# Kernel optimization log

Hardware: AMD Instinct MI355X
Metric: run time of the kernel (lower is better)

Reference implementation:

```python
import jax, jax.numpy as jnp
import numpy as np
from jax import lax

BS = 256

def layer_norm(x, w, b, eps=1e-5):
    mu = jnp.mean(x, axis=-1, keepdims=True)
    var = jnp.mean((x - mu) ** 2, axis=-1, keepdims=True)
    return (x - mu) / jnp.sqrt(var + eps) * w + b

def conv2d(x, w, b):
    y = lax.conv_general_dilated(x, w, (1, 1), 'VALID', dimension_numbers=('NCHW', 'OIHW', 'NCHW'))
    return y + b[None, :, None, None]

def max_pool2(x):
    return lax.reduce_window(x, -jnp.inf, lax.max, (1, 1, 2, 2), (1, 1, 2, 2), 'VALID')

def mha(x, wqkv, bqkv, wo, bo, nheads):
    # x: (L, B, E); torch nn.MultiheadAttention in eval mode (dropout off)
    L, B, E = x.shape
    hd = E // nheads
    qkv = jnp.einsum('lbd,ed->lbe', x, wqkv) + bqkv
    q, k, v = jnp.split(qkv, 3, axis=-1)
    q = q.reshape(L, B, nheads, hd) * (hd ** -0.5)
    k = k.reshape(L, B, nheads, hd)
    v = v.reshape(L, B, nheads, hd)
    att = jax.nn.softmax(jnp.einsum('qbhd,kbhd->bhqk', q, k), axis=-1)
    o = jnp.einsum('bhqk,kbhd->qbhd', att, v).reshape(L, B, E)
    return jnp.einsum('lbe,oe->lbo', o, wo) + bo

def grouped_mha(u, wqkv, bqkv, wo, bo, nheads):
    # u: (G, L, B, E) -- the 16 distinct small MHA blocks batched into one grouped attention
    G, L, B, E = u.shape
    hd = E // nheads
    qkv = jnp.einsum('glbd,ged->glbe', u, wqkv) + bqkv[:, None, None, :]
    q, k, v = jnp.split(qkv, 3, axis=-1)
    q = q.reshape(G, L, B, nheads, hd) * (hd ** -0.5)
    k = k.reshape(G, L, B, nheads, hd)
    v = v.reshape(G, L, B, nheads, hd)
    att = jax.nn.softmax(jnp.einsum('gqbhd,gkbhd->gbhqk', q, k), axis=-1)
    o = jnp.einsum('gbhqk,gkbhd->gqbhd', att, v).reshape(G, L, B, E)
    return jnp.einsum('glbe,goe->glbo', o, wo) + bo[:, None, None, :]

def setup_inputs() -> dict:
    key = jax.random.key(0)
    ks = iter(jax.random.split(key, 40))
    n = lambda shape, s=0.02: jax.random.normal(next(ks), shape, dtype=jnp.float32) * s
    inp = {
        't': jax.random.uniform(next(ks), (BS, 128, 128), dtype=jnp.float32) * 255.0,
        'conv1_w': n((32, 1, 3, 3), 0.1), 'conv1_b': n((32,)),
        'conv2_w': n((32, 32, 3, 3), 0.05), 'conv2_b': n((32,)),
        'expand_w': n((64, 36), 0.05), 'expand_b': n((64,)),
        'mha_wqkv': n((16, 192, 64)), 'mha_bqkv': n((16, 192)),
        'mha_wo': n((16, 64, 64)), 'mha_bo': n((16, 64)),
        'ln1_w': jnp.ones((64,), jnp.float32), 'ln1_b': jnp.zeros((64,), jnp.float32),
        'enc_wqkv': n((3 * 2048, 2048)), 'enc_bqkv': n((3 * 2048,)),
        'enc_wo': n((2048, 2048)), 'enc_bo': n((2048,)),
        'enc_ln1_w': jnp.ones((2048,), jnp.float32), 'enc_ln1_b': jnp.zeros((2048,), jnp.float32),
        'enc_w1': n((2048, 2048)), 'enc_b1': n((2048,)),
        'enc_w2': n((2048, 2048)), 'enc_b2': n((2048,)),
        'enc_ln2_w': jnp.ones((2048,), jnp.float32), 'enc_ln2_b': jnp.zeros((2048,), jnp.float32),
        'f1_w': n((512, 16 * 2048), 0.01), 'f1_b': n((512,)),
        'f2_w': n((128, 512)), 'f2_b': n((128,)),
        'f3_w': n((25, 128)), 'f3_b': n((25,)),
    }
    return inp

def reference(t, conv1_w, conv1_b, conv2_w, conv2_b, expand_w, expand_b,
              mha_wqkv, mha_bqkv, mha_wo, mha_bo, ln1_w, ln1_b,
              enc_wqkv, enc_bqkv, enc_wo, enc_bo, enc_ln1_w, enc_ln1_b,
              enc_w1, enc_b1, enc_w2, enc_b2, enc_ln2_w, enc_ln2_b,
              f1_w, f1_b, f2_w, f2_b, f3_w, f3_b):
    bs = t.shape[0]
    t = t / 255.0
    # 4x4 grid of 32x32 tiles -> (bs*16, 1, 32, 32); replaces the double python loop
    x = t.reshape(bs, 4, 32, 4, 32).transpose(0, 1, 3, 2, 4).reshape(bs * 16, 1, 32, 32)
    u = max_pool2(conv2d(x, conv1_w, conv1_b))   # (bs*16, 32, 15, 15)
    u = max_pool2(conv2d(u, conv2_w, conv2_b))   # (bs*16, 32, 6, 6)
    u = u.reshape(bs * 16, 32, 36)
    u = jax.nn.relu(u @ expand_w.T + expand_b)
    u = u.reshape(16, 32, bs, 64)                 # raw reshape, exactly as in source
    att = grouped_mha(u, mha_wqkv, mha_bqkv, mha_wo, mha_bo, 4)
    u = layer_norm(u + att, ln1_w, ln1_b)         # dropout is identity in eval
    x = u.reshape(16, bs, 2048)
    # TransformerEncoderLayer d_model=2048, nhead=16, post-norm, ReLU FFN (eval)
    a = mha(x, enc_wqkv, enc_bqkv, enc_wo, enc_bo, 16)
    x = layer_norm(x + a, enc_ln1_w, enc_ln1_b)
    ff = jax.nn.relu(x @ enc_w1.T + enc_b1) @ enc_w2.T + enc_b2
    x = layer_norm(x + ff, enc_ln2_w, enc_ln2_b)
    u = x.reshape(bs, 16 * 2048)                  # raw reshape, exactly as in source
    u = jax.nn.relu(u @ f1_w.T + f1_b)
    u = jax.nn.relu(u @ f2_w.T + f2_b)
    return u @ f3_w.T + f3_b
```

## Files before the change

### kernel.cpp

```cpp
#include <hip/hip_runtime.h>


#define EPS 1e-5f

typedef __attribute__((ext_vector_type(8))) short s16x8;
typedef __attribute__((ext_vector_type(4))) float f32x4;

__device__ inline float bf2f(ushort u) {
    union { unsigned u; float f; } x; x.u = ((unsigned)u) << 16; return x.f;
}
__device__ inline ushort f2bf(float f) {
    union { float f; unsigned u; } x; x.f = f;
    unsigned r = x.u + 0x7FFFu + ((x.u >> 16) & 1u);
    return (ushort)(r >> 16);
}
__device__ inline void gload_lds16(const void* g, void* l) {
    __builtin_amdgcn_global_load_lds(
        (const __attribute__((address_space(1))) unsigned int*)g,
        (__attribute__((address_space(3))) unsigned int*)l, 16, 0, 0);
}

__global__ __launch_bounds__(256) void conv1_pool(
    const float* __restrict__ t, const float* __restrict__ w,
    const float* __restrict__ bias, ushort* __restrict__ out)
{
    __shared__ float tile[32][33];
    __shared__ float ws9[288];
    __shared__ float bs[32];
    int n = blockIdx.x, tid = threadIdx.x;
    int b = n >> 4, tt = n & 15, ty = tt >> 2, tx = tt & 3;
    const float* tb = t + (long)b * 16384 + ty * 32 * 128 + tx * 32;
    for (int i = tid; i < 1024; i += 256) {
        int r = i >> 5, cc = i & 31;
        tile[r][cc] = tb[r * 128 + cc] * (1.0f / 255.0f);
    }
    for (int i = tid; i < 288; i += 256) ws9[i] = w[i];
    if (tid < 32) bs[tid] = bias[tid];
    __syncthreads();
    for (int o = tid; o < 7200; o += 256) {
        int c = o / 225, p = o - c * 225;
        int py = p / 15, px = p - py * 15;
        float in[4][4];
        #pragma unroll
        for (int iy = 0; iy < 4; ++iy) {
            #pragma unroll
            for (int ix = 0; ix < 4; ++ix) in[iy][ix] = tile[py * 2 + iy][px * 2 + ix];
        }
        float b0 = bs[c];
        float a00 = b0, a01 = b0, a10 = b0, a11 = b0;
        const float* wc = &ws9[c * 9];
        #pragma unroll
        for (int ky = 0; ky < 3; ++ky) {
            #pragma unroll
            for (int kx = 0; kx < 3; ++kx) {
                float wv = wc[ky * 3 + kx];
                a00 += in[ky][kx] * wv;     a01 += in[ky][kx + 1] * wv;
                a10 += in[ky + 1][kx] * wv; a11 += in[ky + 1][kx + 1] * wv;
            }
        }
        out[(long)n * 7200 + o] = f2bf(fmaxf(fmaxf(a00, a01), fmaxf(a10, a11)));
    }
}

__global__ __launch_bounds__(256) void convw_prep(
    const float* __restrict__ w, ushort* __restrict__ wk)
{
    int i = blockIdx.x * 256 + threadIdx.x;
    if (i >= 9216) return;
    int kz = i >> 10, rem = i & 1023;
    int oc = rem >> 5, ci = rem & 31;
    wk[i] = f2bf(w[oc * 288 + ci * 9 + kz]);
}

__global__ __launch_bounds__(256) void conv2_mfma(
    const ushort* __restrict__ u1, const ushort* __restrict__ wk,
    const float* __restrict__ bias, float* __restrict__ u2)
{
    __shared__ __align__(16) ushort tiles[2][7680];
    __shared__ float hp[2][2376];
    int tid = threadIdx.x;
    int wave = tid >> 6, lane = tid & 63;
    int n0 = blockIdx.x * 2;

    for (int u = tid; u < 1800; u += 256) {
        int img = u / 900, v = u - img * 900;
        int ks = v / 225, pos = v - ks * 225;
        int y = pos / 15, x = pos - y * 15;
        const ushort* src = u1 + (long)(n0 + img) * 7200 + (ks * 8) * 225 + pos;
        union { s16x8 v8; ushort us[8]; } pk;
        #pragma unroll
        for (int j = 0; j < 8; ++j) pk.us[j] = src[j * 225];
        int r = y * 16 + x;
        int chunk = ks ^ ((r >> 1) & 3);
        *(s16x8*)((char*)&tiles[img][0] + r * 64 + (chunk << 4)) = pk.v8;
    }
    __syncthreads();

    int img = wave >> 1, nf = wave & 1;
    int fr = lane & 15, ks4 = lane >> 4;
    int rb[9];
    #pragma unroll
    for (int m = 0; m < 9; ++m) {
        int pos = m * 16 + fr;
        int py = pos / 12, px = pos - py * 12;
        rb[m] = py * 16 + px;
    }
    f32x4 acc[9];
    #pragma unroll
    for (int m = 0; m < 9; ++m) acc[m] = (f32x4){0.f, 0.f, 0.f, 0.f};
    const char* tbase = (const char*)&tiles[img][0];
    #pragma unroll
    for (int kz = 0; kz < 9; ++kz) {
        int ky = kz / 3, kx = kz - ky * 3;
        s16x8 bf = *(const s16x8*)(wk + kz * 1024 + (nf * 16 + fr) * 32 + ks4 * 8);
        #pragma unroll
        for (int m = 0; m < 9; ++m) {
            int r = rb[m] + ky * 16 + kx;
            s16x8 af = *(const s16x8*)(tbase + r * 64 + ((ks4 ^ ((r >> 1) & 3)) << 4));
            acc[m] = __builtin_amdgcn_mfma_f32_16x16x32_bf16(af, bf, acc[m], 0, 0, 0);
        }
    }

    int oc = nf * 16 + fr;
    int cr4 = ks4 * 4;
    #pragma unroll
    for (int m = 0; m < 9; ++m) {
        float v01 = fmaxf(acc[m][0], acc[m][1]);
        float v23 = fmaxf(acc[m][2], acc[m][3]);
        int p0 = m * 16 + cr4;
        int py = p0 / 12, px0 = p0 - py * 12;
        int rowb = py * 6 + (px0 >> 1);
        hp[img][rowb * 33 + oc] = v01;
        hp[img][(rowb + 1) * 33 + oc] = v23;
    }
    __syncthreads();

    for (int u = tid; u < 2304; u += 256) {
        int im = u / 1152, v = u - im * 1152;
        int o = v / 36, opos = v - o * 36;
        int i = opos / 6, jj = opos - i * 6;
        float a = hp[im][((2 * i) * 6 + jj) * 33 + o];
        float b = hp[im][((2 * i + 1) * 6 + jj) * 33 + o];
        u2[(long)(n0 + im) * 1152 + o * 36 + opos] = fmaxf(a, b) + bias[o];
    }
}

__global__ __launch_bounds__(256) void expand_k(
    const float* __restrict__ u2, const float* __restrict__ w,
    const float* __restrict__ bias, float* __restrict__ out)
{
    __shared__ float ws[2304];
    __shared__ float xs[2304];
    __shared__ float bs[64];
    int tid = threadIdx.x;
    long r0 = (long)blockIdx.x * 64;
    const float* src = u2 + r0 * 36;
    for (int i = tid; i < 2304; i += 256) { ws[i] = w[i]; xs[i] = src[i]; }
    if (tid < 64) bs[tid] = bias[tid];
    __syncthreads();
    int row = tid >> 2, qq = tid & 3;
    float x[36];
    #pragma unroll
    for (int k4 = 0; k4 < 36; k4 += 4) *(float4*)&x[k4] = *(const float4*)&xs[row * 36 + k4];
    float res[16];
    #pragma unroll
    for (int eo = 0; eo < 16; ++eo) {
        int e = qq * 16 + eo;
        const float* wr = &ws[e * 36];
        float acc = bs[e];
        #pragma unroll
        for (int k4 = 0; k4 < 36; k4 += 4) {
            float4 wv = *(const float4*)&wr[k4];
            acc += x[k4] * wv.x + x[k4 + 1] * wv.y + x[k4 + 2] * wv.z + x[k4 + 3] * wv.w;
        }
        res[eo] = fmaxf(acc, 0.0f);
    }
    float* orow = out + (r0 + row) * 64 + qq * 16;
    #pragma unroll
    for (int v4 = 0; v4 < 4; ++v4) *(float4*)(orow + v4 * 4) = *(float4*)&res[v4 * 4];
}

template <int BM, int BN, int BK, int TM, int TN, int ACT, int SPLITK>
__global__ __launch_bounds__(256) void gemm_tn(
    const float* __restrict__ A, const float* __restrict__ B,
    const float* __restrict__ bias, float* __restrict__ C,
    int M, int N, int K, int lda, int ldb, int ldc,
    long sA, long sB, long sBias, long sC)
{
    constexpr int NTX = BN / TN;
    constexpr int KG = BK / 4;
    __shared__ float As[BK][BM + 4];
    __shared__ float Bs[BK][BN + 4];
    int tid = threadIdx.x;
    int tx = tid % NTX, ty = tid / NTX;
    int n0 = blockIdx.x * BN, m0 = blockIdx.y * BM;
    int bz = blockIdx.z;
    int batch = bz / SPLITK, kz = bz - batch * SPLITK;
    int Kc = K / SPLITK;
    int k0 = kz * Kc, k1 = k0 + Kc;
    A += (long)batch * sA; B += (long)batch * sB; C += (long)batch * sC;
    const float* bp = bias ? bias + (long)batch * sBias : nullptr;
    float acc[TM][TN] = {};
    for (int kt = k0; kt < k1; kt += BK) {
        constexpr int A4 = BM * BK / 4;
        #pragma unroll
        for (int e0 = 0; e0 < A4; e0 += 256) {
            int e = e0 + tid;
            int rr = e / KG, kg = (e - rr * KG) * 4;
            int gm = m0 + rr;
            float4 v = make_float4(0.f, 0.f, 0.f, 0.f);
            if (gm < M) v = *(const float4*)(A + (long)gm * lda + kt + kg);
            As[kg + 0][rr] = v.x; As[kg + 1][rr] = v.y; As[kg + 2][rr] = v.z; As[kg + 3][rr] = v.w;
        }
        constexpr int B4 = BN * BK / 4;
        #pragma unroll
        for (int e0 = 0; e0 < B4; e0 += 256) {
            int e = e0 + tid;
            int rr = e / KG, kg = (e - rr * KG) * 4;
            int gn = n0 + rr;
            float4 v = make_float4(0.f, 0.f, 0.f, 0.f);
            if (gn < N) v = *(const float4*)(B + (long)gn * ldb + kt + kg);
            Bs[kg + 0][rr] = v.x; Bs[kg + 1][rr] = v.y; Bs[kg + 2][rr] = v.z; Bs[kg + 3][rr] = v.w;
        }
        __syncthreads();
        #pragma unroll
        for (int k = 0; k < BK; ++k) {
            float a[TM], b[TN];
            #pragma unroll
            for (int i = 0; i < TM; i += 4) *(float4*)&a[i] = *(const float4*)&As[k][ty * TM + i];
            #pragma unroll
            for (int j = 0; j < TN; j += 4) *(float4*)&b[j] = *(const float4*)&Bs[k][tx * TN + j];
            #pragma unroll
            for (int i = 0; i < TM; ++i) {
                #pragma unroll
                for (int j = 0; j < TN; ++j) acc[i][j] += a[i] * b[j];
            }
        }
        __syncthreads();
    }
    #pragma unroll
    for (int i = 0; i < TM; ++i) {
        int gm = m0 + ty * TM + i;
        if (gm < M) {
            #pragma unroll
            for (int j = 0; j < TN; ++j) {
                int gn = n0 + tx * TN + j;
                if (gn < N) {
                    float v = acc[i][j];
                    if (SPLITK > 1) {
                        atomicAdd(&C[(long)gm * ldc + gn], v);
                    } else {
                        if (bp) v += bp[gn];
                        if (ACT == 1) v = fmaxf(v, 0.0f);
                        C[(long)gm * ldc + gn] = v;
                    }
                }
            }
        }
    }
}

template <int ACT, int OUT_MODE, int SPLITK = 1>
__global__ __launch_bounds__(256) void gemm_bf16(
    const ushort* __restrict__ A, const ushort* __restrict__ B,
    const float* __restrict__ bias, float* __restrict__ Cf,
    ushort* __restrict__ Cb, int M, int N, int K)
{
    __shared__ __align__(16) ushort As[8192];
    __shared__ __align__(16) ushort Bs[8192];
    int tid = threadIdx.x;
    int wave = tid >> 6, lane = tid & 63;
    int m0 = blockIdx.y * 128, n0 = blockIdx.x * 128;
    const ushort* ga = A + (long)(m0 + wave * 32 + (lane >> 3)) * K + (lane & 7) * 8;
    const ushort* gb = B + (long)(n0 + wave * 32 + (lane >> 3)) * K + (lane & 7) * 8;
    ushort* la = &As[wave * 2048];
    ushort* lb = &Bs[wave * 2048];
    int wr = wave >> 1, wc = wave & 1;
    int fr = lane & 15, ks = (lane >> 4) * 8;
    f32x4 acc[4][4];
    #pragma unroll
    for (int i = 0; i < 4; ++i)
        #pragma unroll
        for (int j = 0; j < 4; ++j) acc[i][j] = (f32x4){0.f, 0.f, 0.f, 0.f};

    int k0 = 0, k1 = K;
    if (SPLITK > 1) { int Kc = K / SPLITK; k0 = blockIdx.z * Kc; k1 = k0 + Kc; }
    for (int kt = k0; kt < k1; kt += 64) {
        #pragma unroll
        for (int i = 0; i < 4; ++i) {
            gload_lds16(ga + kt + (long)i * 8 * K, la + i * 512);
            gload_lds16(gb + kt + (long)i * 8 * K, lb + i * 512);
        }
        __syncthreads();
        #pragma unroll
        for (int kk = 0; kk < 64; kk += 32) {
            s16x8 af[4], bfr[4];
            #pragma unroll
            for (int m = 0; m < 4; ++m)
                af[m] = *(const s16x8*)&As[(wr * 64 + m * 16 + fr) * 64 + kk + ks];
            #pragma unroll
            for (int n = 0; n < 4; ++n)
                bfr[n] = *(const s16x8*)&Bs[(wc * 64 + n * 16 + fr) * 64 + kk + ks];
            #pragma unroll
            for (int m = 0; m < 4; ++m)
                #pragma unroll
                for (int n = 0; n < 4; ++n)
                    acc[m][n] = __builtin_amdgcn_mfma_f32_16x16x32_bf16(
                        af[m], bfr[n], acc[m][n], 0, 0, 0);
        }
        __syncthreads();
    }
    int cr = (lane >> 4) * 4;
    #pragma unroll
    for (int n = 0; n < 4; ++n) {
        int col = n0 + wc * 64 + n * 16 + fr;
        float bv = (SPLITK == 1 && bias) ? bias[col] : 0.f;
        #pragma unroll
        for (int m = 0; m < 4; ++m) {
            #pragma unroll
            for (int j = 0; j < 4; ++j) {
                int row = m0 + wr * 64 + m * 16 + cr + j;
                float v = acc[m][n][j] + bv;
                if (SPLITK > 1) {
                    Cf[(long)blockIdx.z * M * N + (long)row * N + col] = v;
                } else {
                    if (ACT == 1) v = fmaxf(v, 0.f);
                    if (OUT_MODE != 2) Cf[(long)row * N + col] = v;
                    if (OUT_MODE != 0) Cb[(long)row * N + col] = f2bf(v);
                }
            }
        }
    }
}

__global__ __launch_bounds__(256) void f1_reduce(
    const float* __restrict__ part, const float* __restrict__ bias,
    float* __restrict__ out)
{
    int i = blockIdx.x * 256 + threadIdx.x;
    float s = 0.f;
    #pragma unroll 8
    for (int k = 0; k < 64; ++k) s += part[(long)k * 131072 + i];
    out[i] = fmaxf(s + bias[i & 511], 0.f);
}

__global__ __launch_bounds__(256) void f2b_kernel(
    const float* __restrict__ in, ushort* __restrict__ out, int n8)
{
    int i = blockIdx.x * 256 + threadIdx.x;
    if (i >= n8) return;
    long base = (long)i * 8;
    float4 v0 = *(const float4*)(in + base);
    float4 v1 = *(const float4*)(in + base + 4);
    ushort4 a, b;
    a.x = f2bf(v0.x); a.y = f2bf(v0.y); a.z = f2bf(v0.z); a.w = f2bf(v0.w);
    b.x = f2bf(v1.x); b.y = f2bf(v1.y); b.z = f2bf(v1.z); b.w = f2bf(v1.w);
    *(ushort4*)(out + base) = a;
    *(ushort4*)(out + base + 4) = b;
}

__global__ __launch_bounds__(256) void gatt_ln(
    const float* __restrict__ qkv, const float* __restrict__ u,
    const float* __restrict__ wo, const float* __restrict__ bo,
    const float* __restrict__ lnw, const float* __restrict__ lnb,
    ushort* __restrict__ out)
{
    __shared__ float sm[12928];
    float* qs  = sm;
    float* ks  = sm + 2112;
    float* vs  = sm + 4160;
    float* wos = sm + 6208;
    float* os  = sm + 10560;
    float* psT = sm;
    float* bos = sm + 12736;
    float* lws = sm + 12800;
    float* lbs = sm + 12864;
    int gb = blockIdx.x;
    int g = gb >> 8, b = gb & 255;
    int tid = threadIdx.x;

    const float* base = qkv + (long)g * 1572864 + b * 192;
    for (int e = tid; e < 1536; e += 256) {
        int s = e / 48, c4 = (e - s * 48) * 4;
        float4 v = *(const float4*)(base + (long)s * 49152 + c4);
        if (c4 < 64) {
            float* q = &qs[s * 66 + c4];
            q[0] = v.x * 0.25f; q[1] = v.y * 0.25f; q[2] = v.z * 0.25f; q[3] = v.w * 0.25f;
        } else if (c4 < 128) {
            *(float4*)&ks[s * 64 + (c4 - 64)] = v;
        } else {
            *(float4*)&vs[s * 64 + (c4 - 128)] = v;
        }
    }
    const float* wog = wo + g * 4096;
    for (int i = tid; i < 4096; i += 256) wos[(i >> 6) * 68 + (i & 63)] = wog[i];
    if (tid < 64) { bos[tid] = bo[g * 64 + tid]; lws[tid] = lnw[tid]; lbs[tid] = lnb[tid]; }
    __syncthreads();

    int hr = tid >> 1;
    int h = hr >> 5, qi = hr & 31, half = tid & 1;
    float qreg[16];
    #pragma unroll
    for (int d2 = 0; d2 < 16; d2 += 2)
        *(float2*)&qreg[d2] = *(const float2*)&qs[qi * 66 + h * 16 + d2];
    float sc[16];
    #pragma unroll
    for (int jj = 0; jj < 16; ++jj) {
        int j = half * 16 + jj;
        const float* kr = &ks[j * 64 + h * 16];
        float a = 0.f;
        #pragma unroll
        for (int d4 = 0; d4 < 16; d4 += 4) {
            float4 kv = *(const float4*)&kr[d4];
            a += qreg[d4] * kv.x + qreg[d4 + 1] * kv.y + qreg[d4 + 2] * kv.z + qreg[d4 + 3] * kv.w;
        }
        sc[jj] = a;
    }
    float mx = sc[0];
    #pragma unroll
    for (int jj = 1; jj < 16; ++jj) mx = fmaxf(mx, sc[jj]);
    mx = fmaxf(mx, __shfl_xor(mx, 1));
    float sum = 0.f;
    #pragma unroll
    for (int jj = 0; jj < 16; ++jj) { sc[jj] = __expf(sc[jj] - mx); sum += sc[jj]; }
    sum += __shfl_xor(sum, 1);
    float inv = 1.0f / sum;
    __syncthreads();
    #pragma unroll
    for (int jj = 0; jj < 16; ++jj)
        psT[(half * 16 + jj) * 128 + h * 32 + qi] = sc[jj] * inv;
    __syncthreads();

    int si = tid >> 3, e0 = (tid & 7) * 8;
    int hh = e0 >> 4;
    float oacc[8] = {};
    for (int j = 0; j < 32; ++j) {
        float pj = psT[j * 128 + hh * 32 + si];
        const float* vr = &vs[j * 64 + e0];
        float4 v0 = *(const float4*)&vr[0];
        float4 v1 = *(const float4*)&vr[4];
        oacc[0] += pj * v0.x; oacc[1] += pj * v0.y; oacc[2] += pj * v0.z; oacc[3] += pj * v0.w;
        oacc[4] += pj * v1.x; oacc[5] += pj * v1.y; oacc[6] += pj * v1.z; oacc[7] += pj * v1.w;
    }
    #pragma unroll
    for (int e = 0; e < 8; ++e) os[si * 68 + e0 + e] = oacc[e];
    __syncthreads();

    int r8 = tid & 7;
    float z[8];
    {
        float accq[8];
        #pragma unroll
        for (int q = 0; q < 8; ++q) accq[q] = bos[r8 + q * 8];
        #pragma unroll 4
        for (int e4 = 0; e4 < 64; e4 += 4) {
            float4 ov = *(const float4*)&os[si * 68 + e4];
            #pragma unroll
            for (int q = 0; q < 8; ++q) {
                float4 wv = *(const float4*)&wos[(r8 + q * 8) * 68 + e4];
                accq[q] += ov.x * wv.x + ov.y * wv.y + ov.z * wv.z + ov.w * wv.w;
            }
        }
        long ubase = (((long)g * 32 + si) * 256 + b) * 64;
        #pragma unroll
        for (int q = 0; q < 8; ++q) z[q] = accq[q] + u[ubase + r8 + q * 8];
    }
    float s1 = 0.f, s2 = 0.f;
    #pragma unroll
    for (int q = 0; q < 8; ++q) { s1 += z[q]; s2 += z[q] * z[q]; }
    #pragma unroll
    for (int off = 1; off < 8; off <<= 1) { s1 += __shfl_xor(s1, off); s2 += __shfl_xor(s2, off); }
    float mu = s1 * 0.015625f;
    float var = s2 * 0.015625f - mu * mu;
    float rstd = rsqrtf(var + EPS);
    long obase = (((long)g * 32 + si) * 256 + b) * 64;
    #pragma unroll
    for (int q = 0; q < 8; ++q) {
        int e2 = r8 + q * 8;
        out[obase + e2] = f2bf((z[q] - mu) * rstd * lws[e2] + lbs[e2]);
    }
}

__global__ __launch_bounds__(256) void enc_att(
    const float* __restrict__ qkv, ushort* __restrict__ o)
{
    __shared__ float qs[16 * 132], ks[16 * 132], vs[16 * 132], ps[16 * 17];
    int bh = blockIdx.x;
    int b2 = bh >> 4, h = bh & 15;
    int tid = threadIdx.x;
    const float qscale = 0.08838834764831845f;
    for (int e = tid; e < 512; e += 256) {
        int l = e >> 5, c4 = (e & 31) * 4;
        long rowoff = ((long)l * 256 + b2) * 6144 + h * 128 + c4;
        float4 q = *(const float4*)(qkv + rowoff);
        float4 k = *(const float4*)(qkv + rowoff + 2048);
        float4 v = *(const float4*)(qkv + rowoff + 4096);
        q.x *= qscale; q.y *= qscale; q.z *= qscale; q.w *= qscale;
        *(float4*)&qs[l * 132 + c4] = q;
        *(float4*)&ks[l * 132 + c4] = k;
        *(float4*)&vs[l * 132 + c4] = v;
    }
    __syncthreads();
    int qi = tid >> 4, j = tid & 15;
    float acc = 0.f;
    #pragma unroll
    for (int d = 0; d < 128; d += 4) {
        float4 qv = *(const float4*)&qs[qi * 132 + d];
        float4 kv = *(const float4*)&ks[j * 132 + d];
        acc += qv.x * kv.x + qv.y * kv.y + qv.z * kv.z + qv.w * kv.w;
    }
    float m = acc;
    #pragma unroll
    for (int off = 1; off < 16; off <<= 1) m = fmaxf(m, __shfl_xor(m, off));
    float p = __expf(acc - m);
    float sum = p;
    #pragma unroll
    for (int off = 1; off < 16; off <<= 1) sum += __shfl_xor(sum, off);
    ps[qi * 17 + j] = p / sum;
    __syncthreads();
    float pr[16];
    #pragma unroll
    for (int jj = 0; jj < 16; ++jj) pr[jj] = ps[qi * 17 + jj];
    long obase = ((long)qi * 256 + b2) * 2048 + h * 128;
    #pragma unroll
    for (int qd = 0; qd < 8; ++qd) {
        int d = (tid & 15) + qd * 16;
        float a = 0.f;
        #pragma unroll
        for (int jj = 0; jj < 16; ++jj) a += pr[jj] * vs[jj * 132 + d];
        o[obase + d] = f2bf(a);
    }
}

template <int RSD_BF, int OUT_BF>
__global__ __launch_bounds__(256) void resid_ln(
    const float* __restrict__ y, const void* __restrict__ rsdv,
    const float* __restrict__ w, const float* __restrict__ bb,
    float* __restrict__ out, ushort* __restrict__ outb)
{
    __shared__ float red[8];
    int tid = threadIdx.x;
    long row = blockIdx.x;
    const float* yr = y + row * 2048;
    float4 a0 = *(const float4*)(yr + tid * 4);
    float4 a1 = *(const float4*)(yr + 1024 + tid * 4);
    float r[8];
    if (RSD_BF) {
        const ushort* rr = (const ushort*)rsdv + row * 2048;
        ushort4 u0 = *(const ushort4*)(rr + tid * 4);
        ushort4 u1 = *(const ushort4*)(rr + 1024 + tid * 4);
        r[0] = bf2f(u0.x); r[1] = bf2f(u0.y); r[2] = bf2f(u0.z); r[3] = bf2f(u0.w);
        r[4] = bf2f(u1.x); r[5] = bf2f(u1.y); r[6] = bf2f(u1.z); r[7] = bf2f(u1.w);
    } else {
        const float* rr = (const float*)rsdv + row * 2048;
        float4 r0 = *(const float4*)(rr + tid * 4);
        float4 r1 = *(const float4*)(rr + 1024 + tid * 4);
        r[0] = r0.x; r[1] = r0.y; r[2] = r0.z; r[3] = r0.w;
        r[4] = r1.x; r[5] = r1.y; r[6] = r1.z; r[7] = r1.w;
    }
    float v[8] = { a0.x + r[0], a0.y + r[1], a0.z + r[2], a0.w + r[3],
                   a1.x + r[4], a1.y + r[5], a1.z + r[6], a1.w + r[7] };
    float s1 = 0.f, s2 = 0.f;
    #pragma unroll
    for (int i = 0; i < 8; ++i) { s1 += v[i]; s2 += v[i] * v[i]; }
    #pragma unroll
    for (int off = 1; off < 64; off <<= 1) { s1 += __shfl_xor(s1, off); s2 += __shfl_xor(s2, off); }
    int wid = tid >> 6, lane = tid & 63;
    if (lane == 0) { red[wid * 2] = s1; red[wid * 2 + 1] = s2; }
    __syncthreads();
    s1 = red[0] + red[2] + red[4] + red[6];
    s2 = red[1] + red[3] + red[5] + red[7];
    float mu = s1 * (1.0f / 2048.0f);
    float var = s2 * (1.0f / 2048.0f) - mu * mu;
    float rstd = rsqrtf(var + EPS);
    float4 w0 = *(const float4*)(w + tid * 4);
    float4 w1 = *(const float4*)(w + 1024 + tid * 4);
    float4 b0 = *(const float4*)(bb + tid * 4);
    float4 b1 = *(const float4*)(bb + 1024 + tid * 4);
    float o0[8];
    o0[0] = (v[0] - mu) * rstd * w0.x + b0.x; o0[1] = (v[1] - mu) * rstd * w0.y + b0.y;
    o0[2] = (v[2] - mu) * rstd * w0.z + b0.z; o0[3] = (v[3] - mu) * rstd * w0.w + b0.w;
    o0[4] = (v[4] - mu) * rstd * w1.x + b1.x; o0[5] = (v[5] - mu) * rstd * w1.y + b1.y;
    o0[6] = (v[6] - mu) * rstd * w1.z + b1.z; o0[7] = (v[7] - mu) * rstd * w1.w + b1.w;
    *(float4*)(out + row * 2048 + tid * 4) = *(float4*)&o0[0];
    *(float4*)(out + row * 2048 + 1024 + tid * 4) = *(float4*)&o0[4];
    if (OUT_BF) {
        ushort4 q0, q1;
        q0.x = f2bf(o0[0]); q0.y = f2bf(o0[1]); q0.z = f2bf(o0[2]); q0.w = f2bf(o0[3]);
        q1.x = f2bf(o0[4]); q1.y = f2bf(o0[5]); q1.z = f2bf(o0[6]); q1.w = f2bf(o0[7]);
        *(ushort4*)(outb + row * 2048 + tid * 4) = q0;
        *(ushort4*)(outb + row * 2048 + 1024 + tid * 4) = q1;
    }
}

extern "C" void kernel_launch(void* const* d_in, const int* in_sizes, int n_in,
                              void* d_out, int out_size, void* d_ws, size_t ws_size,
                              hipStream_t stream)
{
    (void)in_sizes; (void)n_in; (void)out_size; (void)ws_size;
    const float* t        = (const float*)d_in[0];
    const float* conv1_w  = (const float*)d_in[1];
    const float* conv1_b  = (const float*)d_in[2];
    const float* conv2_w  = (const float*)d_in[3];
    const float* conv2_b  = (const float*)d_in[4];
    const float* expand_w = (const float*)d_in[5];
    const float* expand_b = (const float*)d_in[6];
    const float* mha_wqkv = (const float*)d_in[7];
    const float* mha_bqkv = (const float*)d_in[8];
    const float* mha_wo   = (const float*)d_in[9];
    const float* mha_bo   = (const float*)d_in[10];
    const float* ln1_w    = (const float*)d_in[11];
    const float* ln1_b    = (const float*)d_in[12];
    const float* enc_wqkv = (const float*)d_in[13];
    const float* enc_bqkv = (const float*)d_in[14];
    const float* enc_wo   = (const float*)d_in[15];
    const float* enc_bo   = (const float*)d_in[16];
    const float* enc_ln1w = (const float*)d_in[17];
    const float* enc_ln1b = (const float*)d_in[18];
    const float* enc_w1   = (const float*)d_in[19];
    const float* enc_b1   = (const float*)d_in[20];
    const float* enc_w2   = (const float*)d_in[21];
    const float* enc_b2   = (const float*)d_in[22];
    const float* enc_ln2w = (const float*)d_in[23];
    const float* enc_ln2b = (const float*)d_in[24];
    const float* f1_w     = (const float*)d_in[25];
    const float* f1_b     = (const float*)d_in[26];
    const float* f2_w     = (const float*)d_in[27];
    const float* f2_b     = (const float*)d_in[28];
    const float* f3_w     = (const float*)d_in[29];
    const float* f3_b     = (const float*)d_in[30];
    float* out = (float*)d_out;

    float* W = (float*)d_ws;
    ushort* u1b    = (ushort*)W;
    float*  u2     = W + 29491200;
    float*  u      = W + 34209792;
    float*  qkvg   = W;
    ushort* uln_b  = (ushort*)(W + 42598400);
    ushort* wk     = (ushort*)(W + 46800000);
    ushort* wqkv_b = (ushort*)(W);
    ushort* wo_b   = (ushort*)(W + 6291456);
    ushort* w1_b   = (ushort*)(W + 33554432);
    ushort* w2_b   = (ushort*)(W + 35651584);
    float*  qkv2   = W + 8388608;
    ushort* obuf_b = (ushort*)(W + 37748736);
    float*  ytmp   = W + 8388608;
    float*  x1     = W + 16777216;
    ushort* x1_b   = (ushort*)(W + 25165824);
    ushort* hbuf_b = (ushort*)(W + 29360128);
    float*  x2     = W;
    ushort* x2_b   = (ushort*)(W + 37748736);
    ushort* f1w_b  = (ushort*)(W + 25165824);
    float*  f1part = W + 8388608;
    float*  f1o    = W + 16777216;
    float*  f2o    = W + 16908288;

    dim3 blk(256);
    convw_prep<<<36, blk, 0, stream>>>(conv2_w, wk);
    conv1_pool<<<4096, blk, 0, stream>>>(t, conv1_w, conv1_b, u1b);
    conv2_mfma<<<2048, blk, 0, stream>>>(u1b, wk, conv2_b, u2);
    expand_k<<<2048, blk, 0, stream>>>(u2, expand_w, expand_b, u);
    gemm_tn<64, 64, 16, 4, 4, 0, 1><<<dim3(3, 128, 16), blk, 0, stream>>>(
        u, mha_wqkv, mha_bqkv, qkvg, 8192, 192, 64, 64, 64, 192,
        524288L, 12288L, 192L, 1572864L);
    gatt_ln<<<4096, blk, 0, stream>>>(qkvg, u, mha_wo, mha_bo, ln1_w, ln1_b, uln_b);
    f2b_kernel<<<6144, blk, 0, stream>>>(enc_wqkv, wqkv_b, 1572864);
    f2b_kernel<<<2048, blk, 0, stream>>>(enc_wo, wo_b, 524288);
    f2b_kernel<<<2048, blk, 0, stream>>>(enc_w1, w1_b, 524288);
    f2b_kernel<<<2048, blk, 0, stream>>>(enc_w2, w2_b, 524288);
    gemm_bf16<0, 0><<<dim3(48, 32), blk, 0, stream>>>(
        uln_b, wqkv_b, enc_bqkv, qkv2, nullptr, 4096, 6144, 2048);
    enc_att<<<4096, blk, 0, stream>>>(qkv2, obuf_b);
    gemm_bf16<0, 0><<<dim3(16, 32), blk, 0, stream>>>(
        obuf_b, wo_b, enc_bo, ytmp, nullptr, 4096, 2048, 2048);
    resid_ln<1, 1><<<4096, blk, 0, stream>>>(ytmp, uln_b, enc_ln1w, enc_ln1b, x1, x1_b);
    gemm_bf16<1, 2><<<dim3(16, 32), blk, 0, stream>>>(
        x1_b, w1_b, enc_b1, nullptr, hbuf_b, 4096, 2048, 2048);
    gemm_bf16<0, 0><<<dim3(16, 32), blk, 0, stream>>>(
        hbuf_b, w2_b, enc_b2, ytmp, nullptr, 4096, 2048, 2048);
    resid_ln<0, 1><<<4096, blk, 0, stream>>>(ytmp, x1, enc_ln2w, enc_ln2b, x2, x2_b);
    f2b_kernel<<<8192, blk, 0, stream>>>(f1_w, f1w_b, 2097152);
    gemm_bf16<0, 0, 64><<<dim3(4, 2, 64), blk, 0, stream>>>(
        x2_b, f1w_b, nullptr, f1part, nullptr, 256, 512, 32768);
    f1_reduce<<<512, blk, 0, stream>>>(f1part, f1_b, f1o);
    gemm_tn<64, 64, 16, 4, 4, 1, 1><<<dim3(2, 4, 1), blk, 0, stream>>>(
        f1o, f2_w, f2_b, f2o, 256, 128, 512, 512, 512, 128, 0, 0, 0, 0);
    gemm_tn<64, 64, 16, 4, 4, 0, 1><<<dim3(1, 4, 1), blk, 0, stream>>>(
        f2o, f3_w, f3_b, out, 256, 25, 128, 128, 128, 25, 0, 0, 0, 0);
}
```

Measured before the change: 1.005 ms.

## Use bf16 MFMA for grouped QKV and store intermediate activations in bf16

Replaces the fp32 SIMT grouped QKV GEMM with a bf16 MFMA kernel, fed by a bf16 copy of the expand output and a bf16 copy of the grouped weights. The grouped and encoder QKV outputs are now stored in bf16 and converted back to fp32 in the attention kernels. The second resid_ln no longer writes its unused fp32 output, and the workspace layout is rearranged to fit. This halves the traffic of several large intermediates and moves the small GEMM onto matrix cores, at the cost of extra bf16 rounding in QKV.

```diff
diff --git a/kernel.cpp b/kernel.cpp
--- a/kernel.cpp
+++ b/kernel.cpp
@@ -147,7 +147,8 @@
 
 __global__ __launch_bounds__(256) void expand_k(
     const float* __restrict__ u2, const float* __restrict__ w,
-    const float* __restrict__ bias, float* __restrict__ out)
+    const float* __restrict__ bias, float* __restrict__ out,
+    ushort* __restrict__ outb)
 {
     __shared__ float ws[2304];
     __shared__ float xs[2304];
@@ -176,8 +177,15 @@
         res[eo] = fmaxf(acc, 0.0f);
     }
     float* orow = out + (r0 + row) * 64 + qq * 16;
-    #pragma unroll
-    for (int v4 = 0; v4 < 4; ++v4) *(float4*)(orow + v4 * 4) = *(float4*)&res[v4 * 4];
+    ushort* brow = outb + (r0 + row) * 64 + qq * 16;
+    #pragma unroll
+    for (int v4 = 0; v4 < 4; ++v4) {
+        *(float4*)(orow + v4 * 4) = *(float4*)&res[v4 * 4];
+        ushort4 q;
+        q.x = f2bf(res[v4 * 4 + 0]); q.y = f2bf(res[v4 * 4 + 1]);
+        q.z = f2bf(res[v4 * 4 + 2]); q.w = f2bf(res[v4 * 4 + 3]);
+        *(ushort4*)(brow + v4 * 4) = q;
+    }
 }
 
 template <int BM, int BN, int BK, int TM, int TN, int ACT, int SPLITK>
@@ -333,6 +341,66 @@
     }
 }
 
+__global__ __launch_bounds__(256) void gqkv_mfma(
+    const ushort* __restrict__ A, const ushort* __restrict__ B,
+    const float* __restrict__ bias, ushort* __restrict__ C)
+{
+    __shared__ __align__(16) ushort As[8192];
+    __shared__ __align__(16) ushort Bs[12288];
+    int tid = threadIdx.x;
+    int wave = tid >> 6, lane = tid & 63;
+    int mt = blockIdx.x, g = blockIdx.y;
+    long arow0 = (long)g * 8192 + mt * 128;
+    const ushort* ga = A + (arow0 + wave * 32 + (lane >> 3)) * 64 + (lane & 7) * 8;
+    const ushort* gb = B + (long)g * 12288 + (wave * 48 + (lane >> 3)) * 64 + (lane & 7) * 8;
+    ushort* la = &As[wave * 2048];
+    ushort* lb = &Bs[wave * 3072];
+    #pragma unroll
+    for (int i = 0; i < 4; ++i) gload_lds16(ga + (long)i * 8 * 64, la + i * 512);
+    #pragma unroll
+    for (int i = 0; i < 6; ++i) gload_lds16(gb + (long)i * 8 * 64, lb + i * 512);
+    __syncthreads();
+
+    int wr = wave >> 1, wc = wave & 1;
+    int fr = lane & 15, ks = (lane >> 4) * 8;
+    f32x4 acc[4][6];
+    #pragma unroll
+    for (int m = 0; m < 4; ++m)
+        #pragma unroll
+        for (int n = 0; n < 6; ++n) acc[m][n] = (f32x4){0.f, 0.f, 0.f, 0.f};
+    #pragma unroll
+    for (int kk = 0; kk < 64; kk += 32) {
+        s16x8 af[4], bfr[6];
+        #pragma unroll
+        for (int m = 0; m < 4; ++m)
+            af[m] = *(const s16x8*)&As[(wr * 64 + m * 16 + fr) * 64 + kk + ks];
+        #pragma unroll
+        for (int n = 0; n < 6; ++n)
+            bfr[n] = *(const s16x8*)&Bs[(wc * 96 + n * 16 + fr) * 64 + kk + ks];
+        #pragma unroll
+        for (int m = 0; m < 4; ++m)
+            #pragma unroll
+            for (int n = 0; n < 6; ++n)
+                acc[m][n] = __builtin_amdgcn_mfma_f32_16x16x32_bf16(
+                    af[m], bfr[n], acc[m][n], 0, 0, 0);
+    }
+    int cr = (lane >> 4) * 4;
+    ushort* Cg = C + (long)g * 1572864;
+    #pragma unroll
+    for (int n = 0; n < 6; ++n) {
+        int col = wc * 96 + n * 16 + fr;
+        float bv = bias[g * 192 + col];
+        #pragma unroll
+        for (int m = 0; m < 4; ++m) {
+            #pragma unroll
+            for (int j = 0; j < 4; ++j) {
+                long row = mt * 128 + wr * 64 + m * 16 + cr + j;
+                Cg[row * 192 + col] = f2bf(acc[m][n][j] + bv);
+            }
+        }
+    }
+}
+
 __global__ __launch_bounds__(256) void f1_reduce(
     const float* __restrict__ part, const float* __restrict__ bias,
     float* __restrict__ out)
@@ -360,7 +428,7 @@
 }
 
 __global__ __launch_bounds__(256) void gatt_ln(
-    const float* __restrict__ qkv, const float* __restrict__ u,
+    const ushort* __restrict__ qkv, const float* __restrict__ u,
     const float* __restrict__ wo, const float* __restrict__ bo,
     const float* __restrict__ lnw, const float* __restrict__ lnb,
     ushort* __restrict__ out)
@@ -379,17 +447,23 @@
     int g = gb >> 8, b = gb & 255;
     int tid = threadIdx.x;
 
-    const float* base = qkv + (long)g * 1572864 + b * 192;
-    for (int e = tid; e < 1536; e += 256) {
-        int s = e / 48, c4 = (e - s * 48) * 4;
-        float4 v = *(const float4*)(base + (long)s * 49152 + c4);
-        if (c4 < 64) {
-            float* q = &qs[s * 66 + c4];
-            q[0] = v.x * 0.25f; q[1] = v.y * 0.25f; q[2] = v.z * 0.25f; q[3] = v.w * 0.25f;
-        } else if (c4 < 128) {
-            *(float4*)&ks[s * 64 + (c4 - 64)] = v;
+    const ushort* base = qkv + (long)g * 1572864 + b * 192;
+    for (int e = tid; e < 768; e += 256) {
+        int s = e / 24, c8 = (e % 24) * 8;
+        union { s16x8 v8; ushort us[8]; } pk;
+        pk.v8 = *(const s16x8*)(base + (long)s * 49152 + c8);
+        if (c8 < 64) {
+            float* q = &qs[s * 66 + c8];
+            #pragma unroll
+            for (int j = 0; j < 8; ++j) q[j] = bf2f(pk.us[j]) * 0.25f;
+        } else if (c8 < 128) {
+            float* k = &ks[s * 64 + (c8 - 64)];
+            #pragma unroll
+            for (int j = 0; j < 8; ++j) k[j] = bf2f(pk.us[j]);
         } else {
-            *(float4*)&vs[s * 64 + (c4 - 128)] = v;
+            float* v = &vs[s * 64 + (c8 - 128)];
+            #pragma unroll
+            for (int j = 0; j < 8; ++j) v[j] = bf2f(pk.us[j]);
         }
     }
     const float* wog = wo + g * 4096;
@@ -482,23 +556,27 @@
 }
 
 __global__ __launch_bounds__(256) void enc_att(
-    const float* __restrict__ qkv, ushort* __restrict__ o)
+    const ushort* __restrict__ qkv, ushort* __restrict__ o)
 {
     __shared__ float qs[16 * 132], ks[16 * 132], vs[16 * 132], ps[16 * 17];
     int bh = blockIdx.x;
     int b2 = bh >> 4, h = bh & 15;
     int tid = threadIdx.x;
     const float qscale = 0.08838834764831845f;
-    for (int e = tid; e < 512; e += 256) {
-        int l = e >> 5, c4 = (e & 31) * 4;
-        long rowoff = ((long)l * 256 + b2) * 6144 + h * 128 + c4;
-        float4 q = *(const float4*)(qkv + rowoff);
-        float4 k = *(const float4*)(qkv + rowoff + 2048);
-        float4 v = *(const float4*)(qkv + rowoff + 4096);
-        q.x *= qscale; q.y *= qscale; q.z *= qscale; q.w *= qscale;
-        *(float4*)&qs[l * 132 + c4] = q;
-        *(float4*)&ks[l * 132 + c4] = k;
-        *(float4*)&vs[l * 132 + c4] = v;
+    {
+        int e = tid;
+        int l = e >> 4, c8 = (e & 15) * 8;
+        long rowoff = ((long)l * 256 + b2) * 6144 + h * 128 + c8;
+        union { s16x8 v8; ushort us[8]; } q, k, v;
+        q.v8 = *(const s16x8*)(qkv + rowoff);
+        k.v8 = *(const s16x8*)(qkv + rowoff + 2048);
+        v.v8 = *(const s16x8*)(qkv + rowoff + 4096);
+        #pragma unroll
+        for (int j = 0; j < 8; ++j) {
+            qs[l * 132 + c8 + j] = bf2f(q.us[j]) * qscale;
+            ks[l * 132 + c8 + j] = bf2f(k.us[j]);
+            vs[l * 132 + c8 + j] = bf2f(v.us[j]);
+        }
     }
     __syncthreads();
     int qi = tid >> 4, j = tid & 15;
@@ -582,8 +660,10 @@
     o0[2] = (v[2] - mu) * rstd * w0.z + b0.z; o0[3] = (v[3] - mu) * rstd * w0.w + b0.w;
     o0[4] = (v[4] - mu) * rstd * w1.x + b1.x; o0[5] = (v[5] - mu) * rstd * w1.y + b1.y;
     o0[6] = (v[6] - mu) * rstd * w1.z + b1.z; o0[7] = (v[7] - mu) * rstd * w1.w + b1.w;
-    *(float4*)(out + row * 2048 + tid * 4) = *(float4*)&o0[0];
-    *(float4*)(out + row * 2048 + 1024 + tid * 4) = *(float4*)&o0[4];
+    if (OUT_BF != 2) {
+        *(float4*)(out + row * 2048 + tid * 4) = *(float4*)&o0[0];
+        *(float4*)(out + row * 2048 + 1024 + tid * 4) = *(float4*)&o0[4];
+    }
     if (OUT_BF) {
         ushort4 q0, q1;
         q0.x = f2bf(o0[0]); q0.y = f2bf(o0[1]); q0.z = f2bf(o0[2]); q0.w = f2bf(o0[3]);
@@ -635,42 +715,42 @@
     ushort* u1b    = (ushort*)W;
     float*  u2     = W + 29491200;
     float*  u      = W + 34209792;
-    float*  qkvg   = W;
+    ushort* u_b    = (ushort*)(W + 12582912);
+    ushort* qkvg_b = (ushort*)W;
+    ushort* wqg_b  = (ushort*)(W + 46804608);
     ushort* uln_b  = (ushort*)(W + 42598400);
     ushort* wk     = (ushort*)(W + 46800000);
-    ushort* wqkv_b = (ushort*)(W);
-    ushort* wo_b   = (ushort*)(W + 6291456);
-    ushort* w1_b   = (ushort*)(W + 33554432);
-    ushort* w2_b   = (ushort*)(W + 35651584);
-    float*  qkv2   = W + 8388608;
-    ushort* obuf_b = (ushort*)(W + 37748736);
-    float*  ytmp   = W + 8388608;
-    float*  x1     = W + 16777216;
-    ushort* x1_b   = (ushort*)(W + 25165824);
-    ushort* hbuf_b = (ushort*)(W + 29360128);
-    float*  x2     = W;
-    ushort* x2_b   = (ushort*)(W + 37748736);
-    ushort* f1w_b  = (ushort*)(W + 25165824);
-    float*  f1part = W + 8388608;
-    float*  f1o    = W + 16777216;
-    float*  f2o    = W + 16908288;
+    ushort* wqkv_b = (ushort*)(W + 12582912);
+    ushort* wo_b   = (ushort*)(W + 18874368);
+    ushort* w1_b   = (ushort*)(W + 20971520);
+    ushort* w2_b   = (ushort*)(W + 23068672);
+    ushort* qkv2_b = (ushort*)W;
+    ushort* obuf_b = (ushort*)(W + 25165824);
+    float*  ytmp   = W + 29360128;
+    float*  x1     = W;
+    ushort* x1_b   = (ushort*)(W + 8388608);
+    ushort* hbuf_b = (ushort*)(W + 37748736);
+    ushort* x2_b   = (ushort*)(W + 20971520);
+    ushort* f1w_b  = (ushort*)W;
+    float*  f1part = W + 29360128;
+    float*  f1o    = W + 25165824;
+    float*  f2o    = W + 25296896;
 
     dim3 blk(256);
     convw_prep<<<36, blk, 0, stream>>>(conv2_w, wk);
+    f2b_kernel<<<96, blk, 0, stream>>>(mha_wqkv, wqg_b, 24576);
     conv1_pool<<<4096, blk, 0, stream>>>(t, conv1_w, conv1_b, u1b);
     conv2_mfma<<<2048, blk, 0, stream>>>(u1b, wk, conv2_b, u2);
-    expand_k<<<2048, blk, 0, stream>>>(u2, expand_w, expand_b, u);
-    gemm_tn<64, 64, 16, 4, 4, 0, 1><<<dim3(3, 128, 16), blk, 0, stream>>>(
-        u, mha_wqkv, mha_bqkv, qkvg, 8192, 192, 64, 64, 64, 192,
-        524288L, 12288L, 192L, 1572864L);
-    gatt_ln<<<4096, blk, 0, stream>>>(qkvg, u, mha_wo, mha_bo, ln1_w, ln1_b, uln_b);
+    expand_k<<<2048, blk, 0, stream>>>(u2, expand_w, expand_b, u, u_b);
+    gqkv_mfma<<<dim3(64, 16), blk, 0, stream>>>(u_b, wqg_b, mha_bqkv, qkvg_b);
+    gatt_ln<<<4096, blk, 0, stream>>>(qkvg_b, u, mha_wo, mha_bo, ln1_w, ln1_b, uln_b);
     f2b_kernel<<<6144, blk, 0, stream>>>(enc_wqkv, wqkv_b, 1572864);
     f2b_kernel<<<2048, blk, 0, stream>>>(enc_wo, wo_b, 524288);
     f2b_kernel<<<2048, blk, 0, stream>>>(enc_w1, w1_b, 524288);
     f2b_kernel<<<2048, blk, 0, stream>>>(enc_w2, w2_b, 524288);
-    gemm_bf16<0, 0><<<dim3(48, 32), blk, 0, stream>>>(
-        uln_b, wqkv_b, enc_bqkv, qkv2, nullptr, 4096, 6144, 2048);
-    enc_att<<<4096, blk, 0, stream>>>(qkv2, obuf_b);
+    gemm_bf16<0, 2><<<dim3(48, 32), blk, 0, stream>>>(
+        uln_b, wqkv_b, enc_bqkv, nullptr, qkv2_b, 4096, 6144, 2048);
+    enc_att<<<4096, blk, 0, stream>>>(qkv2_b, obuf_b);
     gemm_bf16<0, 0><<<dim3(16, 32), blk, 0, stream>>>(
         obuf_b, wo_b, enc_bo, ytmp, nullptr, 4096, 2048, 2048);
     resid_ln<1, 1><<<4096, blk, 0, stream>>>(ytmp, uln_b, enc_ln1w, enc_ln1b, x1, x1_b);
@@ -678,7 +758,7 @@
         x1_b, w1_b, enc_b1, nullptr, hbuf_b, 4096, 2048, 2048);
     gemm_bf16<0, 0><<<dim3(16, 32), blk, 0, stream>>>(
         hbuf_b, w2_b, enc_b2, ytmp, nullptr, 4096, 2048, 2048);
-    resid_ln<0, 1><<<4096, blk, 0, stream>>>(ytmp, x1, enc_ln2w, enc_ln2b, x2, x2_b);
+    resid_ln<0, 2><<<4096, blk, 0, stream>>>(ytmp, x1, enc_ln2w, enc_ln2b, nullptr, x2_b);
     f2b_kernel<<<8192, blk, 0, stream>>>(f1_w, f1w_b, 2097152);
     gemm_bf16<0, 0, 64><<<dim3(4, 2, 64), blk, 0, stream>>>(
         x2_b, f1w_b, nullptr, f1part, nullptr, 256, 512, 32768);
```

Result: faster. 944.5 us (-6.0%).
